# Optimization experiments

Measured on AMD Instinct MI355X. Metric: run time of the kernel, lower is better.

The kernel has to match this reference:

```python
import jax, jax.numpy as jnp
import numpy as np

N, D, H = 24, 256, 8
F = D // H  # 32


def setup_inputs() -> dict:
    key = jax.random.key(0)
    ks = jax.random.split(key, 9)
    T = 8192
    x = jax.random.normal(ks[0], (T, N * D), dtype=jnp.float32)
    s = 0.02
    # Joint-specific query weights: (H, N, D, F); shared K/V: (H, D, F)
    Wq = jax.random.normal(ks[1], (H, N, D, F), dtype=jnp.float32) * s
    bq = jax.random.normal(ks[2], (H, N, F), dtype=jnp.float32) * s
    Wk = jax.random.normal(ks[3], (H, D, F), dtype=jnp.float32) * s
    bk = jax.random.normal(ks[4], (H, F), dtype=jnp.float32) * s
    Wv = jax.random.normal(ks[5], (H, D, F), dtype=jnp.float32) * s
    bv = jax.random.normal(ks[6], (H, F), dtype=jnp.float32) * s
    gamma = jnp.ones((N * D,), dtype=jnp.float32)
    beta = jnp.zeros((N * D,), dtype=jnp.float32)
    return {"x": x, "Wq": Wq, "bq": bq, "Wk": Wk, "bk": bk,
            "Wv": Wv, "bv": bv, "gamma": gamma, "beta": beta}


def reference(x, Wq, bq, Wk, bk, Wv, bv, gamma, beta):
    T = x.shape[0]
    xr = x.reshape(T, N, D)                                   # (T, N, D)
    # Shared K/V per head, joint-specific Q per head
    k = jnp.einsum('tnd,hdf->thnf', xr, Wk) + bk[None, :, None, :]
    v = jnp.einsum('tnd,hdf->thnf', xr, Wv) + bv[None, :, None, :]
    q = jnp.einsum('tnd,hndf->thnf', xr, Wq) + bq[None, :, :, :]
    scores = jnp.einsum('thnf,thmf->thnm', q, k) / jnp.sqrt(jnp.float32(F))
    attn = jax.nn.softmax(scores, axis=-1)                    # (T, H, N, N)
    out = jnp.einsum('thnm,thmf->thnf', attn, v)              # (T, H, N, F)
    # Concat heads -> (T, N, H*F) = (T, N, D)
    out = jnp.transpose(out, (0, 2, 1, 3)).reshape(T, N * D)
    # Dropout is identity in eval mode; residual + LayerNorm over N*D
    y = x + out
    mu = jnp.mean(y, axis=-1, keepdims=True)
    var = jnp.mean((y - mu) ** 2, axis=-1, keepdims=True)
    y = (y - mu) * jax.lax.rsqrt(var + 1e-5)
    return y * gamma + beta
```

## Files before the change

### kernel.cpp

```cpp
#include <hip/hip_runtime.h>

#define NT 8192
#define NJ 24
#define DD 256
#define NH 8
#define FF 32
#define C3 768

typedef __attribute__((ext_vector_type(8))) short bf16x8;
typedef __attribute__((ext_vector_type(4))) float f32x4;

__device__ __forceinline__ unsigned short f2bf(float f) {
    union { float f; unsigned int u; } c; c.f = f;
    unsigned int u = c.u;
    unsigned int r = (u + 0x7fffu + ((u >> 16) & 1u)) >> 16;
    return (unsigned short)r;
}
__device__ __forceinline__ float bf2f(unsigned short h) {
    union { unsigned int u; float f; } c; c.u = ((unsigned int)h) << 16;
    return c.f;
}
__device__ __forceinline__ float u2f(unsigned int u) {
    union { unsigned int u; float f; } c; c.u = u;
    return c.f;
}
__device__ __forceinline__ void up8(uint4 w, float* f) {
    f[0] = u2f(w.x << 16); f[1] = u2f(w.x & 0xffff0000u);
    f[2] = u2f(w.y << 16); f[3] = u2f(w.y & 0xffff0000u);
    f[4] = u2f(w.z << 16); f[5] = u2f(w.z & 0xffff0000u);
    f[6] = u2f(w.w << 16); f[7] = u2f(w.w & 0xffff0000u);
}

__global__ void pack_w(const float* __restrict__ Wq, const float* __restrict__ Wk,
                       const float* __restrict__ Wv, unsigned short* __restrict__ wbt) {
    size_t idx = (size_t)blockIdx.x * 256 + threadIdx.x;
    const size_t total = (size_t)NJ * C3 * DD;
    if (idx >= total) return;
    int d = idx & 255;
    int rest = (int)(idx >> 8);
    int c = rest % C3;
    int n = rest / C3;
    float v;
    if (c < 256) {
        int h = c >> 5, f = c & 31;
        v = Wq[((((size_t)h * NJ + n) * DD) + d) * FF + f];
    } else if (c < 512) {
        int cc = c - 256; int h = cc >> 5, f = cc & 31;
        v = Wk[(((size_t)h * DD) + d) * FF + f];
    } else {
        int cc = c - 512; int h = cc >> 5, f = cc & 31;
        v = Wv[(((size_t)h * DD) + d) * FF + f];
    }
    wbt[idx] = f2bf(v);
}

__global__ void pack_b(const float* __restrict__ bq, const float* __restrict__ bk,
                       const float* __restrict__ bv, float* __restrict__ bias) {
    int idx = blockIdx.x * 256 + threadIdx.x;
    if (idx >= NJ * C3) return;
    int c = idx % C3;
    int n = idx / C3;
    float v;
    if (c < 256) {
        int h = c >> 5, f = c & 31;
        v = bq[((h * NJ + n) * FF) + f];
    } else if (c < 512) {
        int cc = c - 256; int h = cc >> 5, f = cc & 31;
        v = bk[h * FF + f];
    } else {
        int cc = c - 512; int h = cc >> 5, f = cc & 31;
        v = bv[h * FF + f];
    }
    bias[idx] = v;
}

__global__ void pack_x(const float* __restrict__ x, unsigned short* __restrict__ xb) {
    size_t idx = (size_t)blockIdx.x * 256 + threadIdx.x;
    const size_t total = (size_t)NT * NJ * DD / 4;
    if (idx >= total) return;
    float4 v = ((const float4*)x)[idx];
    ushort4 h;
    h.x = f2bf(v.x); h.y = f2bf(v.y); h.z = f2bf(v.z); h.w = f2bf(v.w);
    ((ushort4*)xb)[idx] = h;
}

#define BM 128
#define BN 128
#define LDSP 72

__global__ __launch_bounds__(256, 2)
void gemm_qkv(const unsigned short* __restrict__ xb, const unsigned short* __restrict__ wbt,
              const float* __restrict__ bias, unsigned short* __restrict__ qkv,
              int t0) {
    const int nb = blockIdx.x;
    const int mb = blockIdx.y;
    const int nj = blockIdx.z;
    const int tid = threadIdx.x;
    const int wave = tid >> 6, lane = tid & 63;

    __shared__ unsigned short As[BM * LDSP];
    __shared__ unsigned short Bs[BN * LDSP];

    f32x4 acc[4][4];
    #pragma unroll
    for (int i = 0; i < 4; ++i)
        #pragma unroll
        for (int j = 0; j < 4; ++j)
            #pragma unroll
            for (int r = 0; r < 4; ++r) acc[i][j][r] = 0.f;

    const int trow0 = t0 + mb * BM;
    const unsigned short* xA = xb + (size_t)trow0 * (NJ * DD) + nj * DD;
    const unsigned short* wB = wbt + ((size_t)nj * C3 + (size_t)nb * BN) * DD;

    for (int kb = 0; kb < 4; ++kb) {
        {
            const unsigned short* src = xA + kb * 64;
            #pragma unroll
            for (int j = 0; j < 4; ++j) {
                int q = tid + j * 256;
                int row = q >> 3;
                int c8 = (q & 7) * 8;
                int4 v = *(const int4*)(src + (size_t)row * (NJ * DD) + c8);
                *(int4*)&As[row * LDSP + c8] = v;
            }
        }
        {
            const unsigned short* src = wB + kb * 64;
            #pragma unroll
            for (int j = 0; j < 4; ++j) {
                int q = tid + j * 256;
                int row = q >> 3;
                int c8 = (q & 7) * 8;
                int4 v = *(const int4*)(src + (size_t)row * DD + c8);
                *(int4*)&Bs[row * LDSP + c8] = v;
            }
        }
        __syncthreads();
        const int wr = (wave >> 1) * 64;
        const int wc = (wave & 1) * 64;
        const int lr = lane & 15;
        const int kq = (lane >> 4) * 8;
        #pragma unroll
        for (int kk = 0; kk < 2; ++kk) {
            bf16x8 a[4], b[4];
            #pragma unroll
            for (int i = 0; i < 4; ++i)
                a[i] = *(const bf16x8*)&As[(wr + i * 16 + lr) * LDSP + kk * 32 + kq];
            #pragma unroll
            for (int j = 0; j < 4; ++j)
                b[j] = *(const bf16x8*)&Bs[(wc + j * 16 + lr) * LDSP + kk * 32 + kq];
            #pragma unroll
            for (int i = 0; i < 4; ++i)
                #pragma unroll
                for (int j = 0; j < 4; ++j)
                    acc[i][j] = __builtin_amdgcn_mfma_f32_16x16x32_bf16(a[i], b[j], acc[i][j], 0, 0, 0);
        }
        __syncthreads();
    }

    const int wr = (wave >> 1) * 64;
    const int wc = (wave & 1) * 64;
    const int ln = lane & 15;
    const int lq = (lane >> 4) * 4;
    float bv[4];
    #pragma unroll
    for (int j = 0; j < 4; ++j)
        bv[j] = bias[nj * C3 + nb * BN + wc + j * 16 + ln];
    #pragma unroll
    for (int i = 0; i < 4; ++i) {
        #pragma unroll
        for (int r = 0; r < 4; ++r) {
            int trow = mb * BM + wr + i * 16 + lq + r;
            size_t base = ((size_t)trow * NJ + nj) * C3 + (size_t)nb * BN;
            #pragma unroll
            for (int j = 0; j < 4; ++j) {
                float val = acc[i][j][r] + bv[j];
                qkv[base + wc + j * 16 + ln] = f2bf(val);
            }
        }
    }
}

__global__ __launch_bounds__(256, 4)
void attn_ln(const unsigned short* __restrict__ qkv, const float* __restrict__ x,
             const float* __restrict__ gamma, const float* __restrict__ beta,
             float* __restrict__ out, int t0) {
    const int tloc = blockIdx.x;
    const int t = t0 + tloc;
    const int tid = threadIdx.x;
    const int wave = tid >> 6, lane = tid & 63;

    __shared__ __align__(16) char smem[NJ * C3 * 2];
    unsigned short* qs = (unsigned short*)smem;
    float* os = (float*)smem;
    __shared__ float red[8];
    __shared__ float stats[2];

    {
        const int4* src = (const int4*)(qkv + (size_t)tloc * NJ * C3);
        int4* dst = (int4*)qs;
        #pragma unroll
        for (int j = 0; j < 9; ++j)
            dst[tid + j * 256] = src[tid + j * 256];
    }
    __syncthreads();

    float o[FF];
    const bool active = tid < NH * NJ;
    int hn = 0, nn = 0;
    if (active) {
        const int h = tid / NJ;
        const int n = tid - h * NJ;
        hn = h; nn = n;
        const int hb = h * FF;
        float qf[FF];
        {
            const uint4* qp = (const uint4*)(qs + n * C3 + hb);
            #pragma unroll
            for (int jj = 0; jj < 4; ++jj) { uint4 w = qp[jj]; up8(w, &qf[jj * 8]); }
        }
        float s[NJ];
        float mx = -1e30f;
        for (int m = 0; m < NJ; ++m) {
            const uint4* kp = (const uint4*)(qs + m * C3 + 256 + hb);
            float a = 0.f;
            #pragma unroll
            for (int jj = 0; jj < 4; ++jj) {
                uint4 w = kp[jj];
                float kf[8]; up8(w, kf);
                #pragma unroll
                for (int e = 0; e < 8; ++e) a += qf[jj * 8 + e] * kf[e];
            }
            a *= 0.17677669529663687f;
            s[m] = a;
            mx = fmaxf(mx, a);
        }
        float sum = 0.f;
        for (int m = 0; m < NJ; ++m) { s[m] = __expf(s[m] - mx); sum += s[m]; }
        float inv = 1.f / sum;
        #pragma unroll
        for (int f = 0; f < FF; ++f) o[f] = 0.f;
        for (int m = 0; m < NJ; ++m) {
            float w = s[m] * inv;
            const uint4* vp = (const uint4*)(qs + m * C3 + 512 + hb);
            #pragma unroll
            for (int jj = 0; jj < 4; ++jj) {
                uint4 wv = vp[jj];
                float vf[8]; up8(wv, vf);
                #pragma unroll
                for (int e = 0; e < 8; ++e) o[jj * 8 + e] += w * vf[e];
            }
        }
    }
    __syncthreads();
    if (active) {
        float* dst = os + nn * DD + hn * FF;
        #pragma unroll
        for (int jj = 0; jj < 8; ++jj)
            *(float4*)(dst + jj * 4) = make_float4(o[jj * 4], o[jj * 4 + 1], o[jj * 4 + 2], o[jj * 4 + 3]);
    }
    __syncthreads();

    const float4* x4 = (const float4*)(x + (size_t)t * (NJ * DD));
    const float4* o4 = (const float4*)os;
    float4 yv[6];
    float sum = 0.f, sq = 0.f;
    #pragma unroll
    for (int j = 0; j < 6; ++j) {
        float4 a = x4[tid + j * 256];
        float4 b = o4[tid + j * 256];
        float4 y;
        y.x = a.x + b.x; y.y = a.y + b.y; y.z = a.z + b.z; y.w = a.w + b.w;
        yv[j] = y;
        sum += y.x + y.y + y.z + y.w;
        sq  += y.x * y.x + y.y * y.y + y.z * y.z + y.w * y.w;
    }
    #pragma unroll
    for (int off = 32; off > 0; off >>= 1) {
        sum += __shfl_down(sum, off);
        sq  += __shfl_down(sq, off);
    }
    if (lane == 0) { red[wave] = sum; red[4 + wave] = sq; }
    __syncthreads();
    if (tid == 0) {
        float s = red[0] + red[1] + red[2] + red[3];
        float q = red[4] + red[5] + red[6] + red[7];
        float mu = s * (1.f / 6144.f);
        float var = q * (1.f / 6144.f) - mu * mu;
        stats[0] = mu;
        stats[1] = rsqrtf(var + 1e-5f);
    }
    __syncthreads();
    const float mu = stats[0], rs = stats[1];
    const float4* g4 = (const float4*)gamma;
    const float4* b4 = (const float4*)beta;
    float4* out4 = (float4*)(out + (size_t)t * (NJ * DD));
    #pragma unroll
    for (int j = 0; j < 6; ++j) {
        float4 g = g4[tid + j * 256];
        float4 bb = b4[tid + j * 256];
        float4 y = yv[j];
        y.x = (y.x - mu) * rs * g.x + bb.x;
        y.y = (y.y - mu) * rs * g.y + bb.y;
        y.z = (y.z - mu) * rs * g.z + bb.z;
        y.w = (y.w - mu) * rs * g.w + bb.w;
        out4[tid + j * 256] = y;
    }
}

extern "C" void kernel_launch(void* const* d_in, const int* in_sizes, int n_in,
                              void* d_out, int out_size, void* d_ws, size_t ws_size,
                              hipStream_t stream) {
    const float* x     = (const float*)d_in[0];
    const float* Wq    = (const float*)d_in[1];
    const float* bq    = (const float*)d_in[2];
    const float* Wk    = (const float*)d_in[3];
    const float* bk    = (const float*)d_in[4];
    const float* Wv    = (const float*)d_in[5];
    const float* bv    = (const float*)d_in[6];
    const float* gamma = (const float*)d_in[7];
    const float* beta  = (const float*)d_in[8];
    float* out = (float*)d_out;

    char* ws = (char*)d_ws;
    const size_t wbt_bytes  = (size_t)NJ * C3 * DD * 2;
    const size_t bias_bytes = (size_t)NJ * C3 * 4;
    const size_t xb_bytes   = (size_t)NT * NJ * DD * 2;
    unsigned short* wbt = (unsigned short*)ws;
    float* bias = (float*)(ws + wbt_bytes);
    unsigned short* xb  = (unsigned short*)(ws + wbt_bytes + bias_bytes);
    unsigned short* qkv = (unsigned short*)(ws + wbt_bytes + bias_bytes + xb_bytes);

    const size_t fixed = wbt_bytes + bias_bytes + xb_bytes;
    size_t avail = (ws_size > fixed) ? ws_size - fixed : 0;
    int chunk = NT;
    while (chunk > BM && (size_t)chunk * NJ * C3 * 2 > avail) chunk >>= 1;

    const size_t wtotal = (size_t)NJ * C3 * DD;
    pack_w<<<dim3((unsigned)((wtotal + 255) / 256)), dim3(256), 0, stream>>>(Wq, Wk, Wv, wbt);
    pack_b<<<dim3((NJ * C3 + 255) / 256), dim3(256), 0, stream>>>(bq, bk, bv, bias);
    const size_t xtotal4 = (size_t)NT * NJ * DD / 4;
    pack_x<<<dim3((unsigned)((xtotal4 + 255) / 256)), dim3(256), 0, stream>>>(x, xb);

    for (int t0 = 0; t0 < NT; t0 += chunk) {
        gemm_qkv<<<dim3(6, chunk / BM, NJ), dim3(256), 0, stream>>>(xb, wbt, bias, qkv, t0);
        attn_ln<<<dim3(chunk), dim3(256), 0, stream>>>(qkv, x, gamma, beta, out, t0);
    }
}
```

Measured before the change: 678.4 us.

## Stage K/V as fp32 head-major in LDS, load Q directly from global

Result: slower. 710.1 us (+4.7%).

```diff
diff --git a/kernel.cpp b/kernel.cpp
--- a/kernel.cpp
+++ b/kernel.cpp
@@ -182,7 +182,7 @@
     }
 }
 
-__global__ __launch_bounds__(256, 4)
+__global__ __launch_bounds__(256, 3)
 void attn_ln(const unsigned short* __restrict__ qkv, const float* __restrict__ x,
              const float* __restrict__ gamma, const float* __restrict__ beta,
              float* __restrict__ out, int t0) {
@@ -191,65 +191,78 @@
     const int tid = threadIdx.x;
     const int wave = tid >> 6, lane = tid & 63;
 
-    __shared__ __align__(16) char smem[NJ * C3 * 2];
-    unsigned short* qs = (unsigned short*)smem;
-    float* os = (float*)smem;
+    __shared__ __align__(16) float kbuf[NH * NJ * FF];
+    __shared__ __align__(16) float vbuf[NH * NJ * FF];
     __shared__ float red[8];
     __shared__ float stats[2];
+    float* os = kbuf;
 
     {
-        const int4* src = (const int4*)(qkv + (size_t)tloc * NJ * C3);
-        int4* dst = (int4*)qs;
-        #pragma unroll
-        for (int j = 0; j < 9; ++j)
-            dst[tid + j * 256] = src[tid + j * 256];
-    }
-    __syncthreads();
-
-    float o[FF];
+        const uint4* src = (const uint4*)(qkv + (size_t)tloc * NJ * C3);
+        #pragma unroll
+        for (int j = 0; j < 6; ++j) {
+            int idx = tid + j * 256;
+            int m = idx >> 6;
+            int r = idx & 63;
+            uint4 w = src[m * (C3 / 8) + 32 + r];
+            float f[8]; up8(w, f);
+            int c = r * 8;
+            int cc = c & 255;
+            int h = cc >> 5, f0 = cc & 31;
+            float* dst = ((c & 256) ? vbuf : kbuf) + ((h * NJ + m) * FF + f0);
+            *(float4*)dst       = make_float4(f[0], f[1], f[2], f[3]);
+            *(float4*)(dst + 4) = make_float4(f[4], f[5], f[6], f[7]);
+        }
+    }
+
+    float qf[FF];
     const bool active = tid < NH * NJ;
     int hn = 0, nn = 0;
     if (active) {
         const int h = tid / NJ;
         const int n = tid - h * NJ;
         hn = h; nn = n;
-        const int hb = h * FF;
-        float qf[FF];
-        {
-            const uint4* qp = (const uint4*)(qs + n * C3 + hb);
-            #pragma unroll
-            for (int jj = 0; jj < 4; ++jj) { uint4 w = qp[jj]; up8(w, &qf[jj * 8]); }
-        }
+        const uint4* qp = (const uint4*)(qkv + (size_t)tloc * NJ * C3 + n * C3 + h * FF);
+        #pragma unroll
+        for (int jj = 0; jj < 4; ++jj) { uint4 w = qp[jj]; up8(w, &qf[jj * 8]); }
+    }
+    __syncthreads();
+
+    float o[FF];
+    if (active) {
+        const float* Kh = kbuf + hn * (NJ * FF);
+        const float* Vh = vbuf + hn * (NJ * FF);
         float s[NJ];
         float mx = -1e30f;
+        #pragma unroll
         for (int m = 0; m < NJ; ++m) {
-            const uint4* kp = (const uint4*)(qs + m * C3 + 256 + hb);
+            const float4* kp = (const float4*)(Kh + m * FF);
             float a = 0.f;
             #pragma unroll
-            for (int jj = 0; jj < 4; ++jj) {
-                uint4 w = kp[jj];
-                float kf[8]; up8(w, kf);
-                #pragma unroll
-                for (int e = 0; e < 8; ++e) a += qf[jj * 8 + e] * kf[e];
+            for (int jj = 0; jj < 8; ++jj) {
+                float4 k4 = kp[jj];
+                a += qf[jj * 4 + 0] * k4.x + qf[jj * 4 + 1] * k4.y
+                   + qf[jj * 4 + 2] * k4.z + qf[jj * 4 + 3] * k4.w;
             }
             a *= 0.17677669529663687f;
             s[m] = a;
             mx = fmaxf(mx, a);
         }
         float sum = 0.f;
+        #pragma unroll
         for (int m = 0; m < NJ; ++m) { s[m] = __expf(s[m] - mx); sum += s[m]; }
         float inv = 1.f / sum;
         #pragma unroll
         for (int f = 0; f < FF; ++f) o[f] = 0.f;
+        #pragma unroll
         for (int m = 0; m < NJ; ++m) {
             float w = s[m] * inv;
-            const uint4* vp = (const uint4*)(qs + m * C3 + 512 + hb);
-            #pragma unroll
-            for (int jj = 0; jj < 4; ++jj) {
-                uint4 wv = vp[jj];
-                float vf[8]; up8(wv, vf);
-                #pragma unroll
-                for (int e = 0; e < 8; ++e) o[jj * 8 + e] += w * vf[e];
+            const float4* vp = (const float4*)(Vh + m * FF);
+            #pragma unroll
+            for (int jj = 0; jj < 8; ++jj) {
+                float4 v4 = vp[jj];
+                o[jj * 4 + 0] += w * v4.x; o[jj * 4 + 1] += w * v4.y;
+                o[jj * 4 + 2] += w * v4.z; o[jj * 4 + 3] += w * v4.w;
             }
         }
     }
```

## Use direct global-to-LDS loads with XOR swizzle and XCD-aware block remap in QKV GEMM

Applied to the files above, without the earlier changes.

Result: faster. 643.4 us (-5.2%).

```diff
diff --git a/kernel.cpp b/kernel.cpp
--- a/kernel.cpp
+++ b/kernel.cpp
@@ -16,10 +16,6 @@
     unsigned int r = (u + 0x7fffu + ((u >> 16) & 1u)) >> 16;
     return (unsigned short)r;
 }
-__device__ __forceinline__ float bf2f(unsigned short h) {
-    union { unsigned int u; float f; } c; c.u = ((unsigned int)h) << 16;
-    return c.f;
-}
 __device__ __forceinline__ float u2f(unsigned int u) {
     union { unsigned int u; float f; } c; c.u = u;
     return c.f;
@@ -29,6 +25,12 @@
     f[2] = u2f(w.y << 16); f[3] = u2f(w.y & 0xffff0000u);
     f[4] = u2f(w.z << 16); f[5] = u2f(w.z & 0xffff0000u);
     f[6] = u2f(w.w << 16); f[7] = u2f(w.w & 0xffff0000u);
+}
+
+__device__ __forceinline__ void gload16(const void* g, void* l) {
+    __builtin_amdgcn_global_load_lds(
+        (const __attribute__((address_space(1))) unsigned int*)g,
+        (__attribute__((address_space(3))) unsigned int*)l, 16, 0, 0);
 }
 
 __global__ void pack_w(const float* __restrict__ Wq, const float* __restrict__ Wk,
@@ -86,20 +88,25 @@
 
 #define BM 128
 #define BN 128
-#define LDSP 72
-
-__global__ __launch_bounds__(256, 2)
+
+__global__ __launch_bounds__(256, 3)
 void gemm_qkv(const unsigned short* __restrict__ xb, const unsigned short* __restrict__ wbt,
               const float* __restrict__ bias, unsigned short* __restrict__ qkv,
-              int t0) {
-    const int nb = blockIdx.x;
-    const int mb = blockIdx.y;
-    const int nj = blockIdx.z;
+              int t0, int mbs) {
+    const int nwg = gridDim.x;
+    const int cpx = nwg >> 3;
+    const int bid = blockIdx.x;
+    const int swz = (bid & 7) * cpx + (bid >> 3);
+    const int nb = swz % 6;
+    const int rest = swz / 6;
+    const int mb = rest % mbs;
+    const int nj = rest / mbs;
+
     const int tid = threadIdx.x;
     const int wave = tid >> 6, lane = tid & 63;
 
-    __shared__ unsigned short As[BM * LDSP];
-    __shared__ unsigned short Bs[BN * LDSP];
+    __shared__ unsigned short As[BM * 64];
+    __shared__ unsigned short Bs[BN * 64];
 
     f32x4 acc[4][4];
     #pragma unroll
@@ -110,46 +117,47 @@
             for (int r = 0; r < 4; ++r) acc[i][j][r] = 0.f;
 
     const int trow0 = t0 + mb * BM;
-    const unsigned short* xA = xb + (size_t)trow0 * (NJ * DD) + nj * DD;
-    const unsigned short* wB = wbt + ((size_t)nj * C3 + (size_t)nb * BN) * DD;
+    const char* srcA = (const char*)(xb + (size_t)trow0 * (NJ * DD) + nj * DD);
+    const char* srcB = (const char*)(wbt + ((size_t)nj * C3 + (size_t)nb * BN) * DD);
+
+    const int rg = lane >> 3;
+    const int sc = (lane & 7) ^ rg;
+
+    const int wr = (wave >> 1) * 64;
+    const int wc = (wave & 1) * 64;
+    const int lr = lane & 15;
+    const int g  = lane >> 4;
 
     for (int kb = 0; kb < 4; ++kb) {
-        {
-            const unsigned short* src = xA + kb * 64;
-            #pragma unroll
-            for (int j = 0; j < 4; ++j) {
-                int q = tid + j * 256;
-                int row = q >> 3;
-                int c8 = (q & 7) * 8;
-                int4 v = *(const int4*)(src + (size_t)row * (NJ * DD) + c8);
-                *(int4*)&As[row * LDSP + c8] = v;
-            }
-        }
-        {
-            const unsigned short* src = wB + kb * 64;
-            #pragma unroll
-            for (int j = 0; j < 4; ++j) {
-                int q = tid + j * 256;
-                int row = q >> 3;
-                int c8 = (q & 7) * 8;
-                int4 v = *(const int4*)(src + (size_t)row * DD + c8);
-                *(int4*)&Bs[row * LDSP + c8] = v;
-            }
+        #pragma unroll
+        for (int i = 0; i < 4; ++i) {
+            int row0 = wave * 32 + i * 8;
+            gload16(srcA + (size_t)(row0 + rg) * (NJ * DD * 2) + kb * 128 + sc * 16,
+                    (char*)As + row0 * 128);
+        }
+        #pragma unroll
+        for (int i = 0; i < 4; ++i) {
+            int row0 = wave * 32 + i * 8;
+            gload16(srcB + (size_t)(row0 + rg) * (DD * 2) + kb * 128 + sc * 16,
+                    (char*)Bs + row0 * 128);
         }
         __syncthreads();
-        const int wr = (wave >> 1) * 64;
-        const int wc = (wave & 1) * 64;
-        const int lr = lane & 15;
-        const int kq = (lane >> 4) * 8;
+
         #pragma unroll
         for (int kk = 0; kk < 2; ++kk) {
             bf16x8 a[4], b[4];
             #pragma unroll
-            for (int i = 0; i < 4; ++i)
-                a[i] = *(const bf16x8*)&As[(wr + i * 16 + lr) * LDSP + kk * 32 + kq];
-            #pragma unroll
-            for (int j = 0; j < 4; ++j)
-                b[j] = *(const bf16x8*)&Bs[(wc + j * 16 + lr) * LDSP + kk * 32 + kq];
+            for (int i = 0; i < 4; ++i) {
+                int row = wr + i * 16 + lr;
+                int c16 = (kk * 4 + g) ^ (row & 7);
+                a[i] = *(const bf16x8*)((const char*)As + row * 128 + c16 * 16);
+            }
+            #pragma unroll
+            for (int j = 0; j < 4; ++j) {
+                int row = wc + j * 16 + lr;
+                int c16 = (kk * 4 + g) ^ (row & 7);
+                b[j] = *(const bf16x8*)((const char*)Bs + row * 128 + c16 * 16);
+            }
             #pragma unroll
             for (int i = 0; i < 4; ++i)
                 #pragma unroll
@@ -159,8 +167,6 @@
         __syncthreads();
     }
 
-    const int wr = (wave >> 1) * 64;
-    const int wc = (wave & 1) * 64;
     const int ln = lane & 15;
     const int lq = (lane >> 4) * 4;
     float bv[4];
@@ -344,7 +350,8 @@
     pack_x<<<dim3((unsigned)((xtotal4 + 255) / 256)), dim3(256), 0, stream>>>(x, xb);
 
     for (int t0 = 0; t0 < NT; t0 += chunk) {
-        gemm_qkv<<<dim3(6, chunk / BM, NJ), dim3(256), 0, stream>>>(xb, wbt, bias, qkv, t0);
+        int mbs = chunk / BM;
+        gemm_qkv<<<dim3(6 * mbs * NJ), dim3(256), 0, stream>>>(xb, wbt, bias, qkv, t0, mbs);
         attn_ln<<<dim3(chunk), dim3(256), 0, stream>>>(qkv, x, gamma, beta, out, t0);
     }
 }
```
